# Performance work log

Measured on AMD Instinct MI355X. Metric: run time of the kernel, lower is better.

## Reference

```python
import jax, jax.numpy as jnp
import numpy as np

T = 4096  # input sequence length; H = T - 16 after convs+pool


def setup_inputs() -> dict:
    key = jax.random.key(0)
    ks = jax.random.split(key, 20)
    def rn(k, shape, scale=0.05):
        return jax.random.normal(k, shape, dtype=jnp.float32) * scale
    return dict(
        evaluation=rn(ks[0], (T, 128), 1.0),
        template=rn(ks[1], (T, 128), 1.0),
        conv1_w=rn(ks[2], (16, 1, 5, 5)),  conv1_b=rn(ks[3], (16,)),
        conv2_w=rn(ks[4], (32, 16, 5, 5)), conv2_b=rn(ks[5], (32,)),
        conv3_w=rn(ks[6], (64, 32, 5, 5)), conv3_b=rn(ks[7], (64,)),
        lin1_w=rn(ks[8], (64, 3712)),      lin1_b=rn(ks[9], (64,)),
        gru_wih=rn(ks[10], (192, 64)),     gru_whh=rn(ks[11], (192, 64)),
        gru_bih=rn(ks[12], (192,)),        gru_bhh=rn(ks[13], (192,)),
        attn_w=rn(ks[14], (1, 64)),        attn_b=rn(ks[15], (1,)),
        lin3_w=rn(ks[16], (128, 64)),      lin3_b=rn(ks[17], (128,)),
        cls_w=rn(ks[18], (2, 128)),        cls_b=rn(ks[19], (2,)),
    )


def _conv(x, w, b):
    y = jax.lax.conv_general_dilated(x, w, (1, 1), 'VALID',
                                     dimension_numbers=('NCHW', 'OIHW', 'NCHW'))
    return y + b[None, :, None, None]


def _encode(x, c1w, c1b, c2w, c2b, c3w, c3b, l1w, l1b, wih, whh, bih, bhh):
    # x: (T, 128) -> (1, 1, T, 128); no activations between convs (as in source)
    x = x.reshape(1, 1, T, 128)
    x = _conv(x, c1w, c1b)   # (1,16,T-4,124)
    x = _conv(x, c2w, c2b)   # (1,32,T-8,120)
    x = _conv(x, c3w, c3b)   # (1,64,T-12,116)
    x = jax.lax.reduce_window(x, -jnp.inf, jax.lax.max,
                              (1, 1, 5, 2), (1, 1, 1, 2), 'VALID')  # (1,64,H,58)
    H = x.shape[2]
    # faithful raw reshape (channel-major flatten), same as torch.reshape
    x = x.reshape(H, 3712)
    x = x @ l1w.T + l1b      # (H, 64)
    # GRU (torch gate order r,z,n), h0 = 0; input gates precomputed
    gi = x @ wih.T + bih     # (H, 192)
    def step(h, gi_t):
        gh = whh @ h + bhh
        ir, iz, inn = jnp.split(gi_t, 3)
        hr, hz, hn = jnp.split(gh, 3)
        r = jax.nn.sigmoid(ir + hr)
        z = jax.nn.sigmoid(iz + hz)
        n = jnp.tanh(inn + r * hn)
        h_new = (1.0 - z) * n + z * h
        return h_new, h_new
    _, out = jax.lax.scan(step, jnp.zeros((64,), dtype=x.dtype), gi)
    return out               # (H, 64)


def reference(evaluation, template, conv1_w, conv1_b, conv2_w, conv2_b,
              conv3_w, conv3_b, lin1_w, lin1_b, gru_wih, gru_whh, gru_bih,
              gru_bhh, attn_w, attn_b, lin3_w, lin3_b, cls_w, cls_b):
    enc = lambda x: _encode(x, conv1_w, conv1_b, conv2_w, conv2_b, conv3_w,
                            conv3_b, lin1_w, lin1_b, gru_wih, gru_whh,
                            gru_bih, gru_bhh)
    e = enc(evaluation)      # (H, 64)
    t = enc(template)        # (H, 64)
    # alignment: aw[m,n] = <e_m, t_n>, softmax over dim 0 (m)
    aw = jax.nn.softmax(e @ t.T, axis=0)      # (H, H)
    t_prim = aw @ t                            # (H, 64)
    distance = jnp.abs(t_prim - e)             # (H, 64)
    attn = jax.nn.softmax((e @ attn_w.T + attn_b).ravel(), axis=0)  # (H,)
    # NOTE: source loops n over distance.size(dim=1)==64, i.e. only the first
    # 64 rows of distance / first 64 attention weights are used (replicated).
    D = distance.shape[1]
    representation = distance[:D].T @ attn[:D]  # (64,)
    out = jax.nn.relu(representation)
    out = jax.nn.relu(out @ lin3_w.T + lin3_b)
    return out @ cls_w.T + cls_b               # (2,)
```

## Files before the change

### kernel.cpp

```cpp
#include <hip/hip_runtime.h>
#include <hip/hip_fp16.h>

constexpr int T_IN = 4096, W_IN = 128;
constexpr int H1 = 4092, W1 = 124, C1 = 16;
constexpr int H2 = 4088, W2 = 120, C2 = 32;
constexpr int H3 = 4084, W3 = 116, C3 = 64;
constexpr int HP = 4080, WPW = 58;
constexpr int KF = 3712;

typedef float f32x16 __attribute__((ext_vector_type(16)));
typedef _Float16 f16x16 __attribute__((ext_vector_type(16)));
typedef _Float16 half2_t __attribute__((ext_vector_type(2)));

#define LOAD25(SRC, W) \
    float p00=(SRC)[0],        p01=(SRC)[1],        p02=(SRC)[2],        p03=(SRC)[3],        p04=(SRC)[4]; \
    float p10=(SRC)[(W)],      p11=(SRC)[(W)+1],    p12=(SRC)[(W)+2],    p13=(SRC)[(W)+3],    p14=(SRC)[(W)+4]; \
    float p20=(SRC)[2*(W)],    p21=(SRC)[2*(W)+1],  p22=(SRC)[2*(W)+2],  p23=(SRC)[2*(W)+3],  p24=(SRC)[2*(W)+4]; \
    float p30=(SRC)[3*(W)],    p31=(SRC)[3*(W)+1],  p32=(SRC)[3*(W)+2],  p33=(SRC)[3*(W)+3],  p34=(SRC)[3*(W)+4]; \
    float p40=(SRC)[4*(W)],    p41=(SRC)[4*(W)+1],  p42=(SRC)[4*(W)+2],  p43=(SRC)[4*(W)+3],  p44=(SRC)[4*(W)+4];

#define TAPS25(T) \
    T(p00, 0)  T(p01, 1)  T(p02, 2)  T(p03, 3)  T(p04, 4) \
    T(p10, 5)  T(p11, 6)  T(p12, 7)  T(p13, 8)  T(p14, 9) \
    T(p20,10)  T(p21,11)  T(p22,12)  T(p23,13)  T(p24,14) \
    T(p30,15)  T(p31,16)  T(p32,17)  T(p33,18)  T(p34,19) \
    T(p40,20)  T(p41,21)  T(p42,22)  T(p43,23)  T(p44,24)

#define KSTEP16(PK, WPTR) do { \
    const float4* w4_ = (const float4*)(WPTR); \
    float4 wA_ = w4_[0], wB_ = w4_[1], wC_ = w4_[2], wD_ = w4_[3]; \
    a0.x = fmaf((PK), wA_.x, a0.x); a0.y = fmaf((PK), wA_.y, a0.y); \
    a0.z = fmaf((PK), wA_.z, a0.z); a0.w = fmaf((PK), wA_.w, a0.w); \
    a1.x = fmaf((PK), wB_.x, a1.x); a1.y = fmaf((PK), wB_.y, a1.y); \
    a1.z = fmaf((PK), wB_.z, a1.z); a1.w = fmaf((PK), wB_.w, a1.w); \
    a2.x = fmaf((PK), wC_.x, a2.x); a2.y = fmaf((PK), wC_.y, a2.y); \
    a2.z = fmaf((PK), wC_.z, a2.z); a2.w = fmaf((PK), wC_.w, a2.w); \
    a3.x = fmaf((PK), wD_.x, a3.x); a3.y = fmaf((PK), wD_.y, a3.y); \
    a3.z = fmaf((PK), wD_.z, a3.z); a3.w = fmaf((PK), wD_.w, a3.w); \
} while (0)

#define LOAD25H(SRC, W) \
    _Float16 q00=(_Float16)(SRC)[0],      q01=(_Float16)(SRC)[1],      q02=(_Float16)(SRC)[2],      q03=(_Float16)(SRC)[3],      q04=(_Float16)(SRC)[4]; \
    _Float16 q10=(_Float16)(SRC)[(W)],    q11=(_Float16)(SRC)[(W)+1],  q12=(_Float16)(SRC)[(W)+2],  q13=(_Float16)(SRC)[(W)+3],  q14=(_Float16)(SRC)[(W)+4]; \
    _Float16 q20=(_Float16)(SRC)[2*(W)],  q21=(_Float16)(SRC)[2*(W)+1],q22=(_Float16)(SRC)[2*(W)+2],q23=(_Float16)(SRC)[2*(W)+3],q24=(_Float16)(SRC)[2*(W)+4]; \
    _Float16 q30=(_Float16)(SRC)[3*(W)],  q31=(_Float16)(SRC)[3*(W)+1],q32=(_Float16)(SRC)[3*(W)+2],q33=(_Float16)(SRC)[3*(W)+3],q34=(_Float16)(SRC)[3*(W)+4]; \
    _Float16 q40=(_Float16)(SRC)[4*(W)],  q41=(_Float16)(SRC)[4*(W)+1],q42=(_Float16)(SRC)[4*(W)+2],q43=(_Float16)(SRC)[4*(W)+3],q44=(_Float16)(SRC)[4*(W)+4];

#define MKPAIRS() \
    half2_t P0, P1, P2, P3, P4, P5, P6, P7, P8, P9, P10, P11, P12; \
    P0[0]=q00; P0[1]=q01;  P1[0]=q02; P1[1]=q03;  P2[0]=q04; P2[1]=q10; \
    P3[0]=q11; P3[1]=q12;  P4[0]=q13; P4[1]=q14;  P5[0]=q20; P5[1]=q21; \
    P6[0]=q22; P6[1]=q23;  P7[0]=q24; P7[1]=q30;  P8[0]=q31; P8[1]=q32; \
    P9[0]=q33; P9[1]=q34;  P10[0]=q40; P10[1]=q41; P11[0]=q42; P11[1]=q43; \
    P12[0]=q44; P12[1]=(_Float16)0.f;

#define DSTEP16(PH, WPTR) do { \
    const half2_t* wv_ = (const half2_t*)(WPTR); \
    a0.x = __builtin_amdgcn_fdot2((PH), wv_[0],  a0.x, false); \
    a0.y = __builtin_amdgcn_fdot2((PH), wv_[1],  a0.y, false); \
    a0.z = __builtin_amdgcn_fdot2((PH), wv_[2],  a0.z, false); \
    a0.w = __builtin_amdgcn_fdot2((PH), wv_[3],  a0.w, false); \
    a1.x = __builtin_amdgcn_fdot2((PH), wv_[4],  a1.x, false); \
    a1.y = __builtin_amdgcn_fdot2((PH), wv_[5],  a1.y, false); \
    a1.z = __builtin_amdgcn_fdot2((PH), wv_[6],  a1.z, false); \
    a1.w = __builtin_amdgcn_fdot2((PH), wv_[7],  a1.w, false); \
    a2.x = __builtin_amdgcn_fdot2((PH), wv_[8],  a2.x, false); \
    a2.y = __builtin_amdgcn_fdot2((PH), wv_[9],  a2.y, false); \
    a2.z = __builtin_amdgcn_fdot2((PH), wv_[10], a2.z, false); \
    a2.w = __builtin_amdgcn_fdot2((PH), wv_[11], a2.w, false); \
    a3.x = __builtin_amdgcn_fdot2((PH), wv_[12], a3.x, false); \
    a3.y = __builtin_amdgcn_fdot2((PH), wv_[13], a3.y, false); \
    a3.z = __builtin_amdgcn_fdot2((PH), wv_[14], a3.z, false); \
    a3.w = __builtin_amdgcn_fdot2((PH), wv_[15], a3.w, false); \
} while (0)

#define PAIRS13(D, CI, CS, WB) \
    D(P0,  ((CI)*13+ 0)) D(P1,  ((CI)*13+ 1)) D(P2,  ((CI)*13+ 2)) \
    D(P3,  ((CI)*13+ 3)) D(P4,  ((CI)*13+ 4)) D(P5,  ((CI)*13+ 5)) \
    D(P6,  ((CI)*13+ 6)) D(P7,  ((CI)*13+ 7)) D(P8,  ((CI)*13+ 8)) \
    D(P9,  ((CI)*13+ 9)) D(P10, ((CI)*13+10)) D(P11, ((CI)*13+11)) \
    D(P12, ((CI)*13+12))

__global__ __launch_bounds__(256, 2) void conv1_k(const float* __restrict__ x,
        const float* __restrict__ wp, const float* __restrict__ b,
        __half* __restrict__ out) {
    int pos = blockIdx.x * 256 + threadIdx.x;
    if (pos >= H1 * W1) return;
    int h = pos / W1, wi = pos - h * W1;
    const float* src = x + h * W_IN + wi;
    const float4* b4 = (const float4*)b;
    float4 a0 = b4[0], a1 = b4[1], a2 = b4[2], a3 = b4[3];
    LOAD25(src, W_IN);
#define T1(P, K) KSTEP16(P, wp + (K) * 16);
    TAPS25(T1)
#undef T1
#pragma unroll
    for (int i = 0; i < 4; i++) {
        float4 v = (i == 0) ? a0 : (i == 1) ? a1 : (i == 2) ? a2 : a3;
        out[(size_t)(i * 4 + 0) * (H1 * W1) + pos] = __float2half(v.x);
        out[(size_t)(i * 4 + 1) * (H1 * W1) + pos] = __float2half(v.y);
        out[(size_t)(i * 4 + 2) * (H1 * W1) + pos] = __float2half(v.z);
        out[(size_t)(i * 4 + 3) * (H1 * W1) + pos] = __float2half(v.w);
    }
}

__global__ __launch_bounds__(256, 2) void conv2_k(const __half* __restrict__ in,
        const _Float16* __restrict__ wp2, const float* __restrict__ b,
        __half* __restrict__ out) {
    int pos = blockIdx.x * 256 + threadIdx.x;
    if (pos >= H2 * W2) return;
    int co0 = blockIdx.y * 16;
    int h = pos / W2, wi = pos - h * W2;
    const float4* b4 = (const float4*)(b + co0);
    float4 a0 = b4[0], a1 = b4[1], a2 = b4[2], a3 = b4[3];
#pragma unroll 1
    for (int ci = 0; ci < C1; ci++) {
        const __half* src = in + (size_t)ci * (H1 * W1) + h * W1 + wi;
        LOAD25H(src, W1);
        MKPAIRS();
#define D2(PH, QI) DSTEP16(PH, wp2 + ((size_t)(QI) * C2 + co0) * 2);
        PAIRS13(D2, ci, C2, wp2)
#undef D2
    }
#pragma unroll
    for (int i = 0; i < 4; i++) {
        float4 v = (i == 0) ? a0 : (i == 1) ? a1 : (i == 2) ? a2 : a3;
        out[(size_t)(co0 + i * 4 + 0) * (H2 * W2) + pos] = __float2half(v.x);
        out[(size_t)(co0 + i * 4 + 1) * (H2 * W2) + pos] = __float2half(v.y);
        out[(size_t)(co0 + i * 4 + 2) * (H2 * W2) + pos] = __float2half(v.z);
        out[(size_t)(co0 + i * 4 + 3) * (H2 * W2) + pos] = __float2half(v.w);
    }
}

__global__ __launch_bounds__(256, 2) void conv3_k(const __half* __restrict__ in,
        const _Float16* __restrict__ wp2, const float* __restrict__ b,
        __half* __restrict__ out) {
    int pos = blockIdx.x * 256 + threadIdx.x;
    if (pos >= H3 * W3) return;
    int co0 = blockIdx.y * 16;
    int h = pos / W3, wi = pos - h * W3;
    const float4* b4 = (const float4*)(b + co0);
    float4 a0 = b4[0], a1 = b4[1], a2 = b4[2], a3 = b4[3];
#pragma unroll 1
    for (int ci = 0; ci < C2; ci++) {
        const __half* src = in + (size_t)ci * (H2 * W2) + h * W2 + wi;
        LOAD25H(src, W2);
        MKPAIRS();
#define D3(PH, QI) DSTEP16(PH, wp2 + ((size_t)(QI) * C3 + co0) * 2);
        PAIRS13(D3, ci, C3, wp2)
#undef D3
    }
#pragma unroll
    for (int i = 0; i < 4; i++) {
        float4 v = (i == 0) ? a0 : (i == 1) ? a1 : (i == 2) ? a2 : a3;
        out[(size_t)(co0 + i * 4 + 0) * (H3 * W3) + pos] = __float2half(v.x);
        out[(size_t)(co0 + i * 4 + 1) * (H3 * W3) + pos] = __float2half(v.y);
        out[(size_t)(co0 + i * 4 + 2) * (H3 * W3) + pos] = __float2half(v.z);
        out[(size_t)(co0 + i * 4 + 3) * (H3 * W3) + pos] = __float2half(v.w);
    }
}

__global__ __launch_bounds__(256) void pool_k(const __half* __restrict__ in,
        float* __restrict__ out) {
    int idx = blockIdx.x * 256 + threadIdx.x;
    if (idx >= C3 * HP * WPW) return;
    int w = idx % WPW; int rest = idx / WPW; int h = rest % HP; int c = rest / HP;
    const __half* base = in + (size_t)c * (H3 * W3) + (size_t)h * W3 + 2 * w;
    float m = -1e30f;
#pragma unroll
    for (int i = 0; i < 5; i++)
#pragma unroll
        for (int j = 0; j < 2; j++)
            m = fmaxf(m, __half2float(base[(size_t)i * W3 + j]));
    out[idx] = m;
}

__global__ __launch_bounds__(256, 2) void lin1_k(const float* __restrict__ X,
        const float* __restrict__ Wt, float* __restrict__ L) {
    __shared__ alignas(16) float Xs[64][68];
    int tid = threadIdx.x;
    int j = tid & 63, mg = tid >> 6;
    int m0 = blockIdx.x * 64;
    int c0 = blockIdx.y * 15;
    int c1 = (c0 + 15 < 58) ? c0 + 15 : 58;
    float4 la0 = {0.f,0.f,0.f,0.f}, la1 = la0, la2 = la0, la3 = la0;
    for (int cc = c0; cc < c1; cc++) {
        int k0 = cc * 64;
        __syncthreads();
#pragma unroll
        for (int tix = 0; tix < 16; tix++) {
            int idx = tid + tix * 256;
            int mm = idx >> 6, kk = idx & 63;
            int m = m0 + mm;
            Xs[kk][mm] = (m < HP) ? X[(size_t)m * KF + k0 + kk] : 0.f;
        }
        __syncthreads();
#pragma unroll 4
        for (int k = 0; k < 64; k++) {
            float wv = Wt[(size_t)(k0 + k) * 64 + j];
            const float4* xr = (const float4*)&Xs[k][mg * 16];
            float4 x0 = xr[0], x1 = xr[1], x2 = xr[2], x3 = xr[3];
            la0.x = fmaf(x0.x, wv, la0.x); la0.y = fmaf(x0.y, wv, la0.y);
            la0.z = fmaf(x0.z, wv, la0.z); la0.w = fmaf(x0.w, wv, la0.w);
            la1.x = fmaf(x1.x, wv, la1.x); la1.y = fmaf(x1.y, wv, la1.y);
            la1.z = fmaf(x1.z, wv, la1.z); la1.w = fmaf(x1.w, wv, la1.w);
            la2.x = fmaf(x2.x, wv, la2.x); la2.y = fmaf(x2.y, wv, la2.y);
            la2.z = fmaf(x2.z, wv, la2.z); la2.w = fmaf(x2.w, wv, la2.w);
            la3.x = fmaf(x3.x, wv, la3.x); la3.y = fmaf(x3.y, wv, la3.y);
            la3.z = fmaf(x3.z, wv, la3.z); la3.w = fmaf(x3.w, wv, la3.w);
        }
    }
    int mb = m0 + mg * 16;
#define LATOM(C, OFF) { int m = mb + (OFF); if (m < HP) atomicAdd(&L[(size_t)m * 64 + j], (C)); }
    LATOM(la0.x, 0)  LATOM(la0.y, 1)  LATOM(la0.z, 2)  LATOM(la0.w, 3)
    LATOM(la1.x, 4)  LATOM(la1.y, 5)  LATOM(la1.z, 6)  LATOM(la1.w, 7)
    LATOM(la2.x, 8)  LATOM(la2.y, 9)  LATOM(la2.z, 10) LATOM(la2.w, 11)
    LATOM(la3.x, 12) LATOM(la3.y, 13) LATOM(la3.z, 14) LATOM(la3.w, 15)
#undef LATOM
}

__global__ __launch_bounds__(192) void gi_k(const float* __restrict__ L,
        const float* __restrict__ wiht, const float* __restrict__ bc,
        float* __restrict__ gi) {
    __shared__ alignas(16) float Ls[8][64];
    int m0 = blockIdx.x * 8, g = threadIdx.x;
    for (int idx = g; idx < 512; idx += 192) {
        int r = idx >> 6, k = idx & 63;
        Ls[r][k] = L[(size_t)(m0 + r) * 64 + k];
    }
    __syncthreads();
    float bcv = bc[g];
#pragma unroll 1
    for (int r = 0; r < 8; r++) {
        float acc = bcv;
#pragma unroll
        for (int k = 0; k < 64; k++) acc = fmaf(Ls[r][k], wiht[k * 192 + g], acc);
        gi[(size_t)(m0 + r) * 192 + g] = acc;
    }
}

__global__ __launch_bounds__(192, 1) void gru_k(const float* __restrict__ gi0,
        const float* __restrict__ gi1, const _Float16* __restrict__ whh_h,
        const float* __restrict__ bhh, float* __restrict__ e,
        float* __restrict__ t) {
    const float* gi = blockIdx.x ? gi1 : gi0;
    float* out = blockIdx.x ? t : e;
    const int g = threadIdx.x;
    const f16x16* wp = (const f16x16*)(whh_h + (size_t)g * 64);
    f16x16 w0 = wp[0], w1 = wp[1], w2 = wp[2], w3 = wp[3];
    float bh = bhh[g];
    __shared__ alignas(64) _Float16 hs[64];
    __shared__ float Ax[192];
    const f16x16* hsv = (const f16x16*)hs;
    float h = 0.f;
    if (g < 64) hs[g] = (_Float16)0.f;
    __syncthreads();
    float p0 = 0.f, p1 = 0.f, p2 = 0.f;
    if (g < 64) { p0 = gi[g]; p1 = gi[64 + g]; p2 = gi[128 + g]; }
#define LGKM_BARRIER() do { \
    asm volatile("s_waitcnt lgkmcnt(0)" ::: "memory"); \
    __builtin_amdgcn_s_barrier(); \
    asm volatile("" ::: "memory"); \
} while (0)
#define DOT8(W, H, ACC) _Pragma("unroll") \
    for (int i_ = 0; i_ < 8; i_++) { \
        half2_t wa_; wa_[0] = (W)[2*i_]; wa_[1] = (W)[2*i_+1]; \
        half2_t ha_; ha_[0] = (H)[2*i_]; ha_[1] = (H)[2*i_+1]; \
        ACC = __builtin_amdgcn_fdot2(wa_, ha_, ACC, false); \
    }
#pragma unroll 1
    for (int m = 0; m < HP; m++) {
        f16x16 hv0 = hsv[0], hv1 = hsv[1], hv2 = hsv[2], hv3 = hsv[3];
        float c0 = p0, c1 = p1, c2 = p2;
        if (g < 64 && m + 1 < HP) {
            const float* gp = gi + (size_t)(m + 1) * 192;
            p0 = gp[g]; p1 = gp[64 + g]; p2 = gp[128 + g];
        }
        float a0 = 0.f, a1 = 0.f, a2 = 0.f, a3 = 0.f;
        DOT8(w0, hv0, a0)
        DOT8(w1, hv1, a1)
        DOT8(w2, hv2, a2)
        DOT8(w3, hv3, a3)
        float a = (a0 + a1) + (a2 + a3) + bh;
        Ax[g] = a;
        LGKM_BARRIER();
        if (g < 64) {
            float az = Ax[64 + g], an = Ax[128 + g];
            float rg = 1.f / (1.f + __expf(-(c0 + a)));
            float zg = 1.f / (1.f + __expf(-(c1 + az)));
            float pre = c2 + rg * an;
            float ex = __expf(2.f * pre);
            float nn = 1.f - 2.f / (ex + 1.f);
            h = (1.f - zg) * nn + zg * h;
            hs[g] = (_Float16)h;
            out[(size_t)m * 64 + g] = h;
        }
        LGKM_BARRIER();
    }
#undef DOT8
#undef LGKM_BARRIER
}

__global__ __launch_bounds__(256) void astat_k(const float* __restrict__ e,
        const float* __restrict__ t, float* __restrict__ pM,
        float* __restrict__ pZ) {
    __shared__ alignas(16) float Ts[64][68];
    __shared__ float Ms[4][64], Zs[4][64];
    int tid = threadIdx.x;
    int nl = tid & 63, ms = tid >> 6;
    int n0 = blockIdx.x * 64;
#pragma unroll
    for (int i = 0; i < 16; i++) {
        int idx = tid + i * 256;
        int rr = idx >> 6, kk = idx & 63;
        int n = n0 + rr;
        Ts[rr][kk] = (n < HP) ? t[(size_t)n * 64 + kk] : 0.f;
    }
    __syncthreads();
    float M = -1e30f, Z = 0.f;
    int m0 = blockIdx.y * 510;
    const float4* Trow = (const float4*)&Ts[nl][0];
    for (int m = m0 + ms; m < m0 + 510; m += 4) {
        const float4* er = (const float4*)(e + (size_t)m * 64);
        float a0 = 0, a1 = 0, a2 = 0, a3 = 0;
#pragma unroll
        for (int i = 0; i < 16; i++) {
            float4 evv = er[i], tv = Trow[i];
            a0 = fmaf(evv.x, tv.x, a0); a1 = fmaf(evv.y, tv.y, a1);
            a2 = fmaf(evv.z, tv.z, a2); a3 = fmaf(evv.w, tv.w, a3);
        }
        float s = (a0 + a1) + (a2 + a3);
        float nM = fmaxf(M, s);
        Z = Z * __expf(M - nM) + __expf(s - nM);
        M = nM;
    }
    Ms[ms][nl] = M; Zs[ms][nl] = Z;
    __syncthreads();
    if (ms == 0) {
#pragma unroll
        for (int i = 1; i < 4; i++) {
            float m2 = Ms[i][nl], z2 = Zs[i][nl];
            float nM = fmaxf(M, m2);
            Z = Z * __expf(M - nM) + z2 * __expf(m2 - nM);
            M = nM;
        }
        int n = n0 + nl;
        if (n < HP) { pM[(size_t)blockIdx.y * HP + n] = M; pZ[(size_t)blockIdx.y * HP + n] = Z; }
    }
}

__global__ __launch_bounds__(256) void attnlog_k(const float* __restrict__ e,
        const float* __restrict__ aw, const float* __restrict__ ab,
        float* __restrict__ alog) {
    int m = blockIdx.x * 256 + threadIdx.x;
    if (m >= HP) return;
    float acc = ab[0];
    const float4* er = (const float4*)(e + (size_t)m * 64);
    const float4* ar = (const float4*)aw;
#pragma unroll
    for (int i = 0; i < 16; i++) {
        float4 evv = er[i], av = ar[i];
        acc += evv.x * av.x + evv.y * av.y + evv.z * av.z + evv.w * av.w;
    }
    alog[m] = acc;
}

__global__ __launch_bounds__(256) void reduce_k(const float* __restrict__ pM,
        const float* __restrict__ pZ, float* __restrict__ Mn,
        float* __restrict__ Zn, const float* __restrict__ alog,
        float* __restrict__ scal) {
    int tid = threadIdx.x;
    if (blockIdx.x < 16) {
        int n = blockIdx.x * 256 + tid;
        if (n >= HP) return;
        float M = pM[n], Z = pZ[n];
#pragma unroll
        for (int y = 1; y < 8; y++) {
            float m2 = pM[(size_t)y * HP + n], z2 = pZ[(size_t)y * HP + n];
            float nM = fmaxf(M, m2);
            Z = Z * __expf(M - nM) + z2 * __expf(m2 - nM);
            M = nM;
        }
        Mn[n] = M; Zn[n] = Z;
    } else {
        __shared__ float red[256];
        float m = -1e30f;
        for (int i = tid; i < HP; i += 256) m = fmaxf(m, alog[i]);
        red[tid] = m; __syncthreads();
        for (int s = 128; s > 0; s >>= 1) {
            if (tid < s) red[tid] = fmaxf(red[tid], red[tid + s]);
            __syncthreads();
        }
        float Ma = red[0]; __syncthreads();
        float z = 0.f;
        for (int i = tid; i < HP; i += 256) z += __expf(alog[i] - Ma);
        red[tid] = z; __syncthreads();
        for (int s = 128; s > 0; s >>= 1) {
            if (tid < s) red[tid] += red[tid + s];
            __syncthreads();
        }
        if (tid == 0) { scal[0] = Ma; scal[1] = red[0]; }
    }
}

__global__ __launch_bounds__(256) void wmat_k(const float* __restrict__ e,
        const float* __restrict__ t, const float* __restrict__ Mn,
        const float* __restrict__ Zn, float* __restrict__ Wm) {
    __shared__ alignas(16) float Es[64][68];
    int tid = threadIdx.x;
#pragma unroll
    for (int i = 0; i < 16; i++) {
        int idx = tid + i * 256;
        int rr = idx >> 6, kk = idx & 63;
        Es[rr][kk] = e[(size_t)rr * 64 + kk];
    }
    __syncthreads();
    int n = blockIdx.x * 256 + tid;
    if (n >= HP) return;
    float tn[64];
    const float4* tr = (const float4*)(t + (size_t)n * 64);
    float4* tn4 = (float4*)tn;
#pragma unroll
    for (int i = 0; i < 16; i++) tn4[i] = tr[i];
    float mM = Mn[n], iZ = 1.f / Zn[n];
#pragma unroll 1
    for (int m = 0; m < 64; m++) {
        const float4* Er = (const float4*)&Es[m][0];
        float a0 = 0, a1 = 0, a2 = 0, a3 = 0;
#pragma unroll
        for (int i = 0; i < 16; i++) {
            float4 evv = Er[i], tv = tn4[i];
            a0 = fmaf(evv.x, tv.x, a0); a1 = fmaf(evv.y, tv.y, a1);
            a2 = fmaf(evv.z, tv.z, a2); a3 = fmaf(evv.w, tv.w, a3);
        }
        float s = (a0 + a1) + (a2 + a3);
        Wm[(size_t)m * HP + n] = __expf(s - mM) * iZ;
    }
}

__global__ __launch_bounds__(256) void tprim_k(const float* __restrict__ Wm,
        const float* __restrict__ t, float* __restrict__ tp) {
    __shared__ float Ws[64][64];
    __shared__ float Ts[64][64];
    int tid = threadIdx.x;
    int n0 = blockIdx.x * 64;
#pragma unroll
    for (int i = 0; i < 16; i++) {
        int idx = tid + i * 256;
        int r = idx >> 6, c = idx & 63;
        Ws[r][c] = (n0 + c < HP) ? Wm[(size_t)r * HP + n0 + c] : 0.f;
        Ts[r][c] = (n0 + r < HP) ? t[(size_t)(n0 + r) * 64 + c] : 0.f;
    }
    __syncthreads();
    int d = tid & 63, mg = tid >> 6;
    float acc[16];
#pragma unroll
    for (int i = 0; i < 16; i++) acc[i] = 0.f;
    for (int k = 0; k < 64; k++) {
        float tv = Ts[k][d];
#pragma unroll
        for (int mm = 0; mm < 16; mm++) acc[mm] = fmaf(Ws[mg * 16 + mm][k], tv, acc[mm]);
    }
#pragma unroll
    for (int mm = 0; mm < 16; mm++)
        atomicAdd(&tp[(size_t)(mg * 16 + mm) * 64 + d], acc[mm]);
}

__global__ __launch_bounds__(256) void final_k(const float* __restrict__ tp,
        const float* __restrict__ e, const float* __restrict__ alog,
        const float* __restrict__ scal, const float* __restrict__ l3w,
        const float* __restrict__ l3b, const float* __restrict__ cw,
        const float* __restrict__ cb, float* __restrict__ out) {
    __shared__ float r1[64], hid[128];
    int tid = threadIdx.x;
    float Ma = scal[0], iZa = 1.f / scal[1];
    if (tid < 64) {
        float acc = 0.f;
        for (int m = 0; m < 64; m++) {
            float a = __expf(alog[m] - Ma) * iZa;
            acc += fabsf(tp[m * 64 + tid] - e[m * 64 + tid]) * a;
        }
        r1[tid] = fmaxf(acc, 0.f);
    }
    __syncthreads();
    if (tid < 128) {
        float acc = l3b[tid];
        for (int d = 0; d < 64; d++) acc = fmaf(r1[d], l3w[tid * 64 + d], acc);
        hid[tid] = fmaxf(acc, 0.f);
    }
    __syncthreads();
    if (tid < 2) {
        float acc = cb[tid];
        for (int j = 0; j < 128; j++) acc = fmaf(hid[j], cw[tid * 128 + j], acc);
        out[tid] = acc;
    }
}

__global__ __launch_bounds__(256) void transpose_l1w_k(const float* __restrict__ w,
        float* __restrict__ wt) {
    int idx = blockIdx.x * 256 + threadIdx.x;
    if (idx >= KF * 64) return;
    int k = idx >> 6, j = idx & 63;
    wt[idx] = w[(size_t)j * KF + k];
}
__global__ __launch_bounds__(256) void pack_w1_k(const float* __restrict__ w,
        float* __restrict__ wp) {
    int idx = blockIdx.x * 256 + threadIdx.x;
    if (idx >= 400) return;
    int k = idx >> 4, co = idx & 15;
    wp[idx] = w[co * 25 + k];
}
__global__ __launch_bounds__(256) void pack_w2p_k(const float* __restrict__ w,
        _Float16* __restrict__ wp2) {
    int idx = blockIdx.x * 256 + threadIdx.x;
    if (idx >= 16 * 13 * 32) return;
    int co = idx & 31; int rest = idx >> 5;
    int q = rest % 13, ci = rest / 13;
    int t0 = 2 * q, t1 = 2 * q + 1;
    float v0 = (t0 < 25) ? w[co * 400 + ci * 25 + t0] : 0.f;
    float v1 = (t1 < 25) ? w[co * 400 + ci * 25 + t1] : 0.f;
    wp2[(size_t)idx * 2 + 0] = (_Float16)v0;
    wp2[(size_t)idx * 2 + 1] = (_Float16)v1;
}
__global__ __launch_bounds__(256) void pack_w3p_k(const float* __restrict__ w,
        _Float16* __restrict__ wp2) {
    int idx = blockIdx.x * 256 + threadIdx.x;
    if (idx >= 32 * 13 * 64) return;
    int co = idx & 63; int rest = idx >> 6;
    int q = rest % 13, ci = rest / 13;
    int t0 = 2 * q, t1 = 2 * q + 1;
    float v0 = (t0 < 25) ? w[co * 800 + ci * 25 + t0] : 0.f;
    float v1 = (t1 < 25) ? w[co * 800 + ci * 25 + t1] : 0.f;
    wp2[(size_t)idx * 2 + 0] = (_Float16)v0;
    wp2[(size_t)idx * 2 + 1] = (_Float16)v1;
}
__global__ __launch_bounds__(256) void pack_wih_k(const float* __restrict__ wih,
        const float* __restrict__ bih, const float* __restrict__ l1b,
        const float* __restrict__ whh, float* __restrict__ wiht,
        float* __restrict__ bc, _Float16* __restrict__ whh_h) {
    int idx = blockIdx.x * 256 + threadIdx.x;
    if (idx < 12288) {
        int g = idx % 192, k = idx / 192;
        wiht[idx] = wih[g * 64 + k];
        whh_h[idx] = (_Float16)whh[idx];
    }
    if (idx < 192) {
        float acc = bih[idx];
#pragma unroll
        for (int k = 0; k < 64; k++) acc = fmaf(wih[idx * 64 + k], l1b[k], acc);
        bc[idx] = acc;
    }
}

extern "C" void kernel_launch(void* const* d_in, const int* in_sizes, int n_in,
                              void* d_out, int out_size, void* d_ws, size_t ws_size,
                              hipStream_t stream) {
    const float* ev    = (const float*)d_in[0];
    const float* tmpl  = (const float*)d_in[1];
    const float* w1    = (const float*)d_in[2];
    const float* b1    = (const float*)d_in[3];
    const float* w2    = (const float*)d_in[4];
    const float* b2    = (const float*)d_in[5];
    const float* w3    = (const float*)d_in[6];
    const float* b3    = (const float*)d_in[7];
    const float* l1w   = (const float*)d_in[8];
    const float* l1b   = (const float*)d_in[9];
    const float* wih   = (const float*)d_in[10];
    const float* whh   = (const float*)d_in[11];
    const float* bih   = (const float*)d_in[12];
    const float* bhh   = (const float*)d_in[13];
    const float* aw    = (const float*)d_in[14];
    const float* ab    = (const float*)d_in[15];
    const float* l3w   = (const float*)d_in[16];
    const float* l3b   = (const float*)d_in[17];
    const float* cw    = (const float*)d_in[18];
    const float* cb    = (const float*)d_in[19];
    float* out = (float*)d_out;
    (void)in_sizes; (void)n_in; (void)out_size;

    char* ws = (char*)d_ws;
    size_t off = 0;
    auto alloc = [&](size_t bytes) -> char* {
        char* p = ws + off;
        off += (bytes + 255) & ~(size_t)255;
        return p;
    };
    size_t szA = (size_t)C3 * H3 * W3 * 2;
    char*  A    = alloc(szA);
    float* B    = (float*)alloc((size_t)HP * KF * 4);
    float* Wt   = (float*)alloc((size_t)KF * 64 * 4);
    float* w1p  = (float*)alloc(400 * 4);
    _Float16* w2p2 = (_Float16*)alloc(16 * 13 * 32 * 2 * 2);
    _Float16* w3p2 = (_Float16*)alloc(32 * 13 * 64 * 2 * 2);
    float* wiht = (float*)alloc(12288 * 4);
    _Float16* whhh = (_Float16*)alloc(12288 * 2);
    float* bc   = (float*)alloc(256 * 4);
    float* L    = (float*)alloc((size_t)HP * 64 * 4);
    float* gi0  = (float*)alloc((size_t)HP * 192 * 4);
    float* gi1  = (float*)alloc((size_t)HP * 192 * 4);
    float* ebuf = (float*)alloc((size_t)HP * 64 * 4);
    float* tbuf = (float*)alloc((size_t)HP * 64 * 4);
    float* pM   = (float*)alloc((size_t)8 * HP * 4);
    float* pZ   = (float*)alloc((size_t)8 * HP * 4);
    float* Mn   = (float*)alloc(HP * 4);
    float* Zn   = (float*)alloc(HP * 4);
    float* Wm   = (float*)alloc((size_t)64 * HP * 4);
    float* alog = (float*)alloc(HP * 4);
    float* tpm  = (float*)alloc(64 * 64 * 4);
    float* scal = (float*)alloc(256);
    if (off > ws_size) return;

    transpose_l1w_k<<<dim3((KF * 64 + 255) / 256), dim3(256), 0, stream>>>(l1w, Wt);
    pack_w1_k<<<dim3(2), dim3(256), 0, stream>>>(w1, w1p);
    pack_w2p_k<<<dim3((16 * 13 * 32 + 255) / 256), dim3(256), 0, stream>>>(w2, w2p2);
    pack_w3p_k<<<dim3((32 * 13 * 64 + 255) / 256), dim3(256), 0, stream>>>(w3, w3p2);
    pack_wih_k<<<dim3(48), dim3(256), 0, stream>>>(wih, bih, l1b, whh, wiht, bc, whhh);

    for (int bsel = 0; bsel < 2; bsel++) {
        const float* xin = bsel ? tmpl : ev;
        float* gib = bsel ? gi1 : gi0;
        conv1_k<<<dim3((H1 * W1 + 255) / 256), dim3(256), 0, stream>>>(xin, w1p, b1, (__half*)A);
        conv2_k<<<dim3((H2 * W2 + 255) / 256, 2), dim3(256), 0, stream>>>((const __half*)A, w2p2, b2, (__half*)B);
        conv3_k<<<dim3((H3 * W3 + 255) / 256, 4), dim3(256), 0, stream>>>((const __half*)B, w3p2, b3, (__half*)A);
        pool_k<<<dim3((C3 * HP * WPW + 255) / 256), dim3(256), 0, stream>>>((const __half*)A, B);
        hipMemsetAsync(L, 0, (size_t)HP * 64 * 4, stream);
        lin1_k<<<dim3(64, 4), dim3(256), 0, stream>>>(B, Wt, L);
        gi_k<<<dim3(HP / 8), dim3(192), 0, stream>>>(L, wiht, bc, gib);
    }
    gru_k<<<dim3(2), dim3(192), 0, stream>>>(gi0, gi1, whhh, bhh, ebuf, tbuf);
    astat_k<<<dim3(64, 8), dim3(256), 0, stream>>>(ebuf, tbuf, pM, pZ);
    attnlog_k<<<dim3(16), dim3(256), 0, stream>>>(ebuf, aw, ab, alog);
    reduce_k<<<dim3(17), dim3(256), 0, stream>>>(pM, pZ, Mn, Zn, alog, scal);
    wmat_k<<<dim3(16), dim3(256), 0, stream>>>(ebuf, tbuf, Mn, Zn, Wm);
    hipMemsetAsync(tpm, 0, 64 * 64 * 4, stream);
    tprim_k<<<dim3(64), dim3(256), 0, stream>>>(Wm, tbuf, tpm);
    final_k<<<dim3(1), dim3(256), 0, stream>>>(tpm, ebuf, alog, scal, l3w, l3b, cw, cb, out);
}
```

Measured before the change: 3.671 ms.

## Run GRU recurrence in a single wavefront, computing all gates per lane

```diff
diff --git a/kernel.cpp b/kernel.cpp
--- a/kernel.cpp
+++ b/kernel.cpp
@@ -74,7 +74,7 @@
     a3.w = __builtin_amdgcn_fdot2((PH), wv_[15], a3.w, false); \
 } while (0)
 
-#define PAIRS13(D, CI, CS, WB) \
+#define PAIRS13(D, CI) \
     D(P0,  ((CI)*13+ 0)) D(P1,  ((CI)*13+ 1)) D(P2,  ((CI)*13+ 2)) \
     D(P3,  ((CI)*13+ 3)) D(P4,  ((CI)*13+ 4)) D(P5,  ((CI)*13+ 5)) \
     D(P6,  ((CI)*13+ 6)) D(P7,  ((CI)*13+ 7)) D(P8,  ((CI)*13+ 8)) \
@@ -119,7 +119,7 @@
         LOAD25H(src, W1);
         MKPAIRS();
 #define D2(PH, QI) DSTEP16(PH, wp2 + ((size_t)(QI) * C2 + co0) * 2);
-        PAIRS13(D2, ci, C2, wp2)
+        PAIRS13(D2, ci)
 #undef D2
     }
 #pragma unroll
@@ -147,7 +147,7 @@
         LOAD25H(src, W2);
         MKPAIRS();
 #define D3(PH, QI) DSTEP16(PH, wp2 + ((size_t)(QI) * C3 + co0) * 2);
-        PAIRS13(D3, ci, C3, wp2)
+        PAIRS13(D3, ci)
 #undef D3
     }
 #pragma unroll
@@ -239,29 +239,26 @@
     }
 }
 
-__global__ __launch_bounds__(192, 1) void gru_k(const float* __restrict__ gi0,
+__global__ __launch_bounds__(64, 1) void gru_k(const float* __restrict__ gi0,
         const float* __restrict__ gi1, const _Float16* __restrict__ whh_h,
         const float* __restrict__ bhh, float* __restrict__ e,
         float* __restrict__ t) {
     const float* gi = blockIdx.x ? gi1 : gi0;
     float* out = blockIdx.x ? t : e;
-    const int g = threadIdx.x;
-    const f16x16* wp = (const f16x16*)(whh_h + (size_t)g * 64);
-    f16x16 w0 = wp[0], w1 = wp[1], w2 = wp[2], w3 = wp[3];
-    float bh = bhh[g];
+    const int l = threadIdx.x;
+    const f16x16* wrp = (const f16x16*)(whh_h + (size_t)l * 64);
+    const f16x16* wzp = (const f16x16*)(whh_h + (size_t)(64 + l) * 64);
+    const f16x16* wnp = (const f16x16*)(whh_h + (size_t)(128 + l) * 64);
+    f16x16 wr0 = wrp[0], wr1 = wrp[1], wr2 = wrp[2], wr3 = wrp[3];
+    f16x16 wz0 = wzp[0], wz1 = wzp[1], wz2 = wzp[2], wz3 = wzp[3];
+    f16x16 wn0 = wnp[0], wn1 = wnp[1], wn2 = wnp[2], wn3 = wnp[3];
+    float bhr = bhh[l], bhz = bhh[64 + l], bhn = bhh[128 + l];
     __shared__ alignas(64) _Float16 hs[64];
-    __shared__ float Ax[192];
     const f16x16* hsv = (const f16x16*)hs;
     float h = 0.f;
-    if (g < 64) hs[g] = (_Float16)0.f;
-    __syncthreads();
-    float p0 = 0.f, p1 = 0.f, p2 = 0.f;
-    if (g < 64) { p0 = gi[g]; p1 = gi[64 + g]; p2 = gi[128 + g]; }
-#define LGKM_BARRIER() do { \
-    asm volatile("s_waitcnt lgkmcnt(0)" ::: "memory"); \
-    __builtin_amdgcn_s_barrier(); \
-    asm volatile("" ::: "memory"); \
-} while (0)
+    hs[l] = (_Float16)0.f;
+    asm volatile("" ::: "memory");
+    float p0 = gi[l], p1 = gi[64 + l], p2 = gi[128 + l];
 #define DOT8(W, H, ACC) _Pragma("unroll") \
     for (int i_ = 0; i_ < 8; i_++) { \
         half2_t wa_; wa_[0] = (W)[2*i_]; wa_[1] = (W)[2*i_+1]; \
@@ -272,33 +269,30 @@
     for (int m = 0; m < HP; m++) {
         f16x16 hv0 = hsv[0], hv1 = hsv[1], hv2 = hsv[2], hv3 = hsv[3];
         float c0 = p0, c1 = p1, c2 = p2;
-        if (g < 64 && m + 1 < HP) {
+        if (m + 1 < HP) {
             const float* gp = gi + (size_t)(m + 1) * 192;
-            p0 = gp[g]; p1 = gp[64 + g]; p2 = gp[128 + g];
-        }
-        float a0 = 0.f, a1 = 0.f, a2 = 0.f, a3 = 0.f;
-        DOT8(w0, hv0, a0)
-        DOT8(w1, hv1, a1)
-        DOT8(w2, hv2, a2)
-        DOT8(w3, hv3, a3)
-        float a = (a0 + a1) + (a2 + a3) + bh;
-        Ax[g] = a;
-        LGKM_BARRIER();
-        if (g < 64) {
-            float az = Ax[64 + g], an = Ax[128 + g];
-            float rg = 1.f / (1.f + __expf(-(c0 + a)));
-            float zg = 1.f / (1.f + __expf(-(c1 + az)));
-            float pre = c2 + rg * an;
-            float ex = __expf(2.f * pre);
-            float nn = 1.f - 2.f / (ex + 1.f);
-            h = (1.f - zg) * nn + zg * h;
-            hs[g] = (_Float16)h;
-            out[(size_t)m * 64 + g] = h;
-        }
-        LGKM_BARRIER();
+            p0 = gp[l]; p1 = gp[64 + l]; p2 = gp[128 + l];
+        }
+        float ar0 = 0.f, ar1 = 0.f, ar2 = 0.f, ar3 = 0.f;
+        float az0 = 0.f, az1 = 0.f, az2 = 0.f, az3 = 0.f;
+        float an0 = 0.f, an1 = 0.f, an2 = 0.f, an3 = 0.f;
+        DOT8(wr0, hv0, ar0) DOT8(wr1, hv1, ar1) DOT8(wr2, hv2, ar2) DOT8(wr3, hv3, ar3)
+        DOT8(wz0, hv0, az0) DOT8(wz1, hv1, az1) DOT8(wz2, hv2, az2) DOT8(wz3, hv3, az3)
+        DOT8(wn0, hv0, an0) DOT8(wn1, hv1, an1) DOT8(wn2, hv2, an2) DOT8(wn3, hv3, an3)
+        float ar = (ar0 + ar1) + (ar2 + ar3) + bhr;
+        float az = (az0 + az1) + (az2 + az3) + bhz;
+        float an = (an0 + an1) + (an2 + an3) + bhn;
+        float rg = 1.f / (1.f + __expf(-(c0 + ar)));
+        float zg = 1.f / (1.f + __expf(-(c1 + az)));
+        float pre = c2 + rg * an;
+        float ex = __expf(2.f * pre);
+        float nn = 1.f - 2.f / (ex + 1.f);
+        h = (1.f - zg) * nn + zg * h;
+        hs[l] = (_Float16)h;
+        asm volatile("" ::: "memory");
+        out[(size_t)m * 64 + l] = h;
     }
 #undef DOT8
-#undef LGKM_BARRIER
 }
 
 __global__ __launch_bounds__(256) void astat_k(const float* __restrict__ e,
@@ -627,7 +621,7 @@
         lin1_k<<<dim3(64, 4), dim3(256), 0, stream>>>(B, Wt, L);
         gi_k<<<dim3(HP / 8), dim3(192), 0, stream>>>(L, wiht, bc, gib);
     }
-    gru_k<<<dim3(2), dim3(192), 0, stream>>>(gi0, gi1, whhh, bhh, ebuf, tbuf);
+    gru_k<<<dim3(2), dim3(64), 0, stream>>>(gi0, gi1, whhh, bhh, ebuf, tbuf);
     astat_k<<<dim3(64, 8), dim3(256), 0, stream>>>(ebuf, tbuf, pM, pZ);
     attnlog_k<<<dim3(16), dim3(256), 0, stream>>>(ebuf, aw, ab, alog);
     reduce_k<<<dim3(17), dim3(256), 0, stream>>>(pM, pZ, Mn, Zn, alog, scal);
```

Result: slower. 4.191 ms (+14.2%).
